# Kernel optimization log

Measured on AMD Instinct MI355X. Metric: run time of the kernel, lower is better.

Reference implementation:

```python
import jax, jax.numpy as jnp
import numpy as np

B, N, D = 8, 1024, 1024
H = 16
HD = D // H  # 64
SCALE = float(HD) ** -0.5


def setup_inputs() -> dict:
    key = jax.random.key(0)
    k1, k2, k3 = jax.random.split(key, 3)
    x = jax.random.normal(k1, (B, N, D), dtype=jnp.float32)
    W_qkv = jax.random.normal(k2, (D, 3 * D), dtype=jnp.float32) * (D ** -0.5)
    b_qkv = jnp.zeros((3 * D,), dtype=jnp.float32)
    W_o = jax.random.normal(k3, (D, D), dtype=jnp.float32) * (D ** -0.5)
    b_o = jnp.zeros((D,), dtype=jnp.float32)
    return {"x": x, "W_qkv": W_qkv, "b_qkv": b_qkv, "W_o": W_o, "b_o": b_o}


def reference(x, W_qkv, b_qkv, W_o, b_o):
    b, n, _ = x.shape
    qkv = x @ W_qkv + b_qkv                      # (B, N, 3D)
    qkv = qkv.reshape(b, n, H, 3 * HD).transpose(0, 2, 1, 3)  # (B, H, N, 3*HD)
    q, k, v = jnp.split(qkv, 3, axis=-1)          # each (B, H, N, HD)
    attn = jnp.einsum('bhnd,bhmd->bhnm', q, k) * SCALE
    attn = jax.nn.softmax(attn, axis=-1)          # (B, H, N, N); dropout p=0 -> identity
    heads = jnp.einsum('bhnm,bhmd->bhnd', attn, v)
    heads = heads.transpose(0, 2, 1, 3).reshape(b, n, H * HD)  # (B, N, D)
    return heads @ W_o + b_o
```

## Files before the change

### kernel.cpp

```cpp
#include <hip/hip_runtime.h>
#include <hip/hip_bf16.h>

typedef unsigned short ushort_t;
typedef __bf16 bf16x8 __attribute__((ext_vector_type(8)));
typedef float floatx4 __attribute__((ext_vector_type(4)));

#define MFMA(a, b, c) __builtin_amdgcn_mfma_f32_16x16x32_bf16(a, b, c, 0, 0, 0)

__device__ __forceinline__ float b2f(ushort_t u) {
    union { ushort_t u; __hip_bfloat16 h; } cvt; cvt.u = u; return __bfloat162float(cvt.h);
}
__device__ __forceinline__ ushort_t f2b(float f) {
    union { ushort_t u; __hip_bfloat16 h; } cvt; cvt.h = __float2bfloat16(f); return cvt.u;
}

__device__ __forceinline__ void async_copy16(const ushort_t* g, ushort_t* l) {
    __builtin_amdgcn_global_load_lds(
        (const __attribute__((address_space(1))) void*)g,
        (__attribute__((address_space(3))) void*)l, 16, 0, 0);
}

__global__ void convert_x(const float* __restrict__ xin, ushort_t* __restrict__ xb) {
    int i = blockIdx.x * 256 + threadIdx.x;
    const float4* xf = (const float4*)xin;
    float4 a = xf[i * 2], b = xf[i * 2 + 1];
    union { ushort_t s[8]; uint4 v; } p;
    p.s[0] = f2b(a.x); p.s[1] = f2b(a.y); p.s[2] = f2b(a.z); p.s[3] = f2b(a.w);
    p.s[4] = f2b(b.x); p.s[5] = f2b(b.y); p.s[6] = f2b(b.z); p.s[7] = f2b(b.w);
    ((uint4*)xb)[i] = p.v;
}

__global__ void transpose_cvt_qkv(const float* __restrict__ W, ushort_t* __restrict__ Wt) {
    __shared__ float tile[32][33];
    int p0 = blockIdx.x * 32, k0 = blockIdx.y * 32;
    int which = p0 >> 10, rem = p0 & 1023;
    int n0 = (rem >> 6) * 192 + which * 64 + (rem & 63);
    int tx = threadIdx.x, ty = threadIdx.y;
#pragma unroll
    for (int i = 0; i < 4; ++i)
        tile[ty + i * 8][tx] = W[(size_t)(k0 + ty + i * 8) * 3072 + n0 + tx];
    __syncthreads();
#pragma unroll
    for (int i = 0; i < 4; ++i)
        Wt[(size_t)(p0 + ty + i * 8) * 1024 + k0 + tx] = f2b(tile[tx][ty + i * 8]);
}

__global__ void transpose_cvt(const float* __restrict__ W, ushort_t* __restrict__ Wt,
                              int K, int N) {
    __shared__ float tile[32][33];
    int n0 = blockIdx.x * 32, k0 = blockIdx.y * 32;
    int tx = threadIdx.x, ty = threadIdx.y;
#pragma unroll
    for (int i = 0; i < 4; ++i)
        tile[ty + i * 8][tx] = W[(size_t)(k0 + ty + i * 8) * N + n0 + tx];
    __syncthreads();
#pragma unroll
    for (int i = 0; i < 4; ++i)
        Wt[(size_t)(n0 + ty + i * 8) * K + k0 + tx] = f2b(tile[tx][ty + i * 8]);
}

__device__ __forceinline__ int tswz(int n, int m) {
    return n * 128 + (((m >> 3) ^ (n & 15)) << 3) + (m & 7);
}

__global__ __launch_bounds__(256, 3) void gemm_qkv(
    const ushort_t* __restrict__ A,
    const ushort_t* __restrict__ Bt,
    const float* __restrict__ bias,
    ushort_t* __restrict__ Qb, ushort_t* __restrict__ Kb, ushort_t* __restrict__ Vtb) {
    const int K = 1024;
    __shared__ __align__(16) ushort_t SH[16384];
    ushort_t* Alds = SH;
    ushort_t* Blds = SH + 8192;
    int tid = threadIdx.x;
    int wave = tid >> 6, lane = tid & 63;
    int quad = lane >> 4, l16 = lane & 15;
    int wm = (wave >> 1) * 64, wn = (wave & 1) * 64;
    int m0 = blockIdx.x * 128, n0 = blockIdx.y * 128;

    floatx4 acc[4][4] = {};

    int srow[4], scol[4];
#pragma unroll
    for (int p = 0; p < 4; ++p) {
        int slot = (wave * 4 + p) * 64 + lane;
        int row = slot >> 3;
        srow[p] = row;
        scol[p] = ((slot & 7) ^ (row & 7)) * 8;
    }

    for (int kt = 0; kt < 16; ++kt) {
        int k0 = kt * 64;
        __syncthreads();
#pragma unroll
        for (int p = 0; p < 4; ++p) {
            int t = wave * 4 + p;
            async_copy16(&A[(m0 + srow[p]) * K + k0 + scol[p]], &Alds[t * 512]);
            async_copy16(&Bt[(n0 + srow[p]) * K + k0 + scol[p]], &Blds[t * 512]);
        }
        __syncthreads();
#pragma unroll
        for (int ki = 0; ki < 2; ++ki) {
            bf16x8 af[4], bfv[4];
            int sc = ((ki * 4 + quad) ^ (l16 & 7)) * 8;
#pragma unroll
            for (int i = 0; i < 4; ++i) {
                __builtin_memcpy(&af[i],  &Alds[(wm + i * 16 + l16) * 64 + sc], 16);
                __builtin_memcpy(&bfv[i], &Blds[(wn + i * 16 + l16) * 64 + sc], 16);
            }
#pragma unroll
            for (int i = 0; i < 4; ++i)
#pragma unroll
                for (int j = 0; j < 4; ++j)
                    acc[i][j] = MFMA(af[i], bfv[j], acc[i][j]);
        }
    }

    int which = n0 >> 10;
    int b = m0 >> 10;

    if (which < 2) {
        ushort_t* dst = which ? Kb : Qb;
        float sc = which ? 1.0f : 0.18033688f;
#pragma unroll
        for (int j = 0; j < 4; ++j) {
            int C = n0 + wn + j * 16 + l16;
            int c = C & 1023;
            int h = c >> 6, d = c & 63;
            float bv = bias[((C >> 6) & 15) * 192 + which * 64 + (C & 63)];
            size_t hb = (size_t)(b * 16 + h) * 65536 + d;
#pragma unroll
            for (int i = 0; i < 4; ++i)
#pragma unroll
                for (int g = 0; g < 4; ++g) {
                    int n_tok = (m0 & 1023) + wm + i * 16 + quad * 4 + g;
                    dst[hb + (size_t)n_tok * 64] = f2b((acc[i][j][g] + bv) * sc);
                }
        }
    } else {
        __syncthreads();
#pragma unroll
        for (int j = 0; j < 4; ++j) {
            int C = n0 + wn + j * 16 + l16;
            int nl = wn + j * 16 + l16;
            float bv = bias[((C >> 6) & 15) * 192 + 128 + (C & 63)];
#pragma unroll
            for (int i = 0; i < 4; ++i)
#pragma unroll
                for (int g = 0; g < 4; ++g) {
                    int ml = wm + i * 16 + quad * 4 + g;
                    SH[tswz(nl, ml)] = f2b(acc[i][j][g] + bv);
                }
        }
        __syncthreads();
        int r = tid >> 1, half = tid & 1;
        int vcol = (n0 - 2048) + r;
        int h = vcol >> 6, d = vcol & 63;
        size_t base = ((size_t)(b * 16 + h) * 64 + d) * 1024 + (m0 & 1023) + half * 64;
#pragma unroll
        for (int i8 = 0; i8 < 8; ++i8) {
            int chunk = half * 8 + i8;
            uint4 v;
            __builtin_memcpy(&v, &SH[r * 128 + ((chunk ^ (r & 15)) << 3)], 16);
            __builtin_memcpy(&Vtb[base + i8 * 8], &v, 16);
        }
    }
}

__global__ __launch_bounds__(256, 3) void attn(
    const ushort_t* __restrict__ Qb, const ushort_t* __restrict__ Kb,
    const ushort_t* __restrict__ Vtb, ushort_t* __restrict__ heads) {
    __shared__ __align__(16) ushort_t Klds[2][4096];
    __shared__ __align__(16) ushort_t Vlds[2][4096];
    __shared__ __align__(16) ushort_t Plds[128 * 76];
    int tid = threadIdx.x;
    int wave = tid >> 6, lane = tid & 63;
    int quad = lane >> 4, l16 = lane & 15;

    int slot = blockIdx.y + 16 * blockIdx.z;
    int bh = blockIdx.x + 8 * (slot >> 3);
    int qx = slot & 7;
    int b = bh >> 4, h = bh & 15;
    const ushort_t* Qh = Qb + (size_t)bh * 65536;
    const ushort_t* Kh = Kb + (size_t)bh * 65536;
    const ushort_t* Vh = Vtb + (size_t)bh * 65536;

    bf16x8 qa[2][2];
#pragma unroll
    for (int mi = 0; mi < 2; ++mi) {
        int qrow = qx * 128 + wave * 32 + mi * 16 + l16;
        __builtin_memcpy(&qa[mi][0], &Qh[qrow * 64 + quad * 8], 16);
        __builtin_memcpy(&qa[mi][1], &Qh[qrow * 64 + 32 + quad * 8], 16);
    }

    floatx4 oacc[2][4] = {};
    floatx4 oext[2] = {};

    bf16x8 onesfrag;
    {
        ushort_t v = (l16 == 0) ? (ushort_t)0x3F80 : (ushort_t)0;
        ushort_t tmp[8] = {v, v, v, v, v, v, v, v};
        __builtin_memcpy(&onesfrag, tmp, 16);
    }

    int srow[2], scol[2];
#pragma unroll
    for (int p = 0; p < 2; ++p) {
        int slot2 = (wave * 2 + p) * 64 + lane;
        int row = slot2 >> 3;
        srow[p] = row;
        scol[p] = ((slot2 & 7) ^ (row & 7)) * 8;
    }

#pragma unroll
    for (int p = 0; p < 2; ++p) {
        int t = wave * 2 + p;
        async_copy16(&Kh[srow[p] * 64 + scol[p]], &Klds[0][t * 512]);
        async_copy16(&Vh[srow[p] * 1024 + scol[p]], &Vlds[0][t * 512]);
    }

    for (int kt = 0; kt < 16; ++kt) {
        int cur = kt & 1;
        __syncthreads();
        if (kt < 15) {
            int nk0 = (kt + 1) * 64, nb = cur ^ 1;
#pragma unroll
            for (int p = 0; p < 2; ++p) {
                int t = wave * 2 + p;
                async_copy16(&Kh[(nk0 + srow[p]) * 64 + scol[p]], &Klds[nb][t * 512]);
                async_copy16(&Vh[srow[p] * 1024 + nk0 + scol[p]], &Vlds[nb][t * 512]);
            }
        }

        bf16x8 kf[4][2];
#pragma unroll
        for (int n = 0; n < 4; ++n)
#pragma unroll
            for (int ki = 0; ki < 2; ++ki) {
                int sc = ((ki * 4 + quad) ^ (l16 & 7)) * 8;
                __builtin_memcpy(&kf[n][ki], &Klds[cur][(n * 16 + l16) * 64 + sc], 16);
            }
#pragma unroll
        for (int mi = 0; mi < 2; ++mi)
#pragma unroll
            for (int n = 0; n < 4; ++n) {
                floatx4 z = {0.f, 0.f, 0.f, 0.f};
#pragma unroll
                for (int ki = 0; ki < 2; ++ki)
                    z = MFMA(kf[n][ki], qa[mi][ki], z);
                union { ushort_t s[4]; double d8; } pk;
#pragma unroll
                for (int g = 0; g < 4; ++g)
                    pk.s[g] = f2b(__builtin_exp2f(z[g]));
                __builtin_memcpy(
                    &Plds[(wave * 32 + mi * 16 + l16) * 76 + n * 16 + quad * 4],
                    &pk, 8);
            }

        bf16x8 vf[4][2];
#pragma unroll
        for (int n = 0; n < 4; ++n)
#pragma unroll
            for (int ki = 0; ki < 2; ++ki) {
                int sc = ((ki * 4 + quad) ^ (l16 & 7)) * 8;
                __builtin_memcpy(&vf[n][ki], &Vlds[cur][(n * 16 + l16) * 64 + sc], 16);
            }
#pragma unroll
        for (int mi = 0; mi < 2; ++mi) {
            bf16x8 pa[2];
            int prow = wave * 32 + mi * 16 + l16;
#pragma unroll
            for (int ki = 0; ki < 2; ++ki)
                __builtin_memcpy(&pa[ki], &Plds[prow * 76 + ki * 32 + quad * 8], 16);
            __builtin_amdgcn_s_setprio(1);
#pragma unroll
            for (int n = 0; n < 4; ++n)
#pragma unroll
                for (int ki = 0; ki < 2; ++ki)
                    oacc[mi][n] = MFMA(pa[ki], vf[n][ki], oacc[mi][n]);
#pragma unroll
            for (int ki = 0; ki < 2; ++ki)
                oext[mi] = MFMA(pa[ki], onesfrag, oext[mi]);
            __builtin_amdgcn_s_setprio(0);
        }
    }

#pragma unroll
    for (int mi = 0; mi < 2; ++mi)
#pragma unroll
        for (int g = 0; g < 4; ++g) {
            float l = __shfl(oext[mi][g], (lane & 48));
            float inv = 1.f / l;
            int n_tok = qx * 128 + wave * 32 + mi * 16 + quad * 4 + g;
#pragma unroll
            for (int n = 0; n < 4; ++n)
                heads[(size_t)(b * 1024 + n_tok) * 1024 + h * 64 + n * 16 + l16] =
                    f2b(oacc[mi][n][g] * inv);
        }
}

__global__ __launch_bounds__(256, 3) void gemm_out(
    const ushort_t* __restrict__ A,
    const ushort_t* __restrict__ Bt,
    const float* __restrict__ bias,
    float* __restrict__ out) {
    const int K = 1024;
    __shared__ __align__(16) ushort_t Alds[128 * 64];
    __shared__ __align__(16) ushort_t Blds[128 * 64];
    int tid = threadIdx.x;
    int wave = tid >> 6, lane = tid & 63;
    int quad = lane >> 4, l16 = lane & 15;
    int wm = (wave >> 1) * 64, wn = (wave & 1) * 64;
    int m0 = blockIdx.x * 128, n0 = blockIdx.y * 128;

    floatx4 acc[4][4] = {};

    int srow[4], scol[4];
#pragma unroll
    for (int p = 0; p < 4; ++p) {
        int slot = (wave * 4 + p) * 64 + lane;
        int row = slot >> 3;
        srow[p] = row;
        scol[p] = ((slot & 7) ^ (row & 7)) * 8;
    }

    for (int kt = 0; kt < 16; ++kt) {
        int k0 = kt * 64;
        __syncthreads();
#pragma unroll
        for (int p = 0; p < 4; ++p) {
            int t = wave * 4 + p;
            async_copy16(&A[(m0 + srow[p]) * K + k0 + scol[p]], &Alds[t * 512]);
            async_copy16(&Bt[(n0 + srow[p]) * K + k0 + scol[p]], &Blds[t * 512]);
        }
        __syncthreads();
#pragma unroll
        for (int ki = 0; ki < 2; ++ki) {
            bf16x8 af[4], bfv[4];
            int sc = ((ki * 4 + quad) ^ (l16 & 7)) * 8;
#pragma unroll
            for (int i = 0; i < 4; ++i) {
                __builtin_memcpy(&af[i],  &Alds[(wm + i * 16 + l16) * 64 + sc], 16);
                __builtin_memcpy(&bfv[i], &Blds[(wn + i * 16 + l16) * 64 + sc], 16);
            }
#pragma unroll
            for (int i = 0; i < 4; ++i)
#pragma unroll
                for (int j = 0; j < 4; ++j)
                    acc[i][j] = MFMA(af[i], bfv[j], acc[i][j]);
        }
    }

#pragma unroll
    for (int j = 0; j < 4; ++j) {
        int C = n0 + wn + j * 16 + l16;
        float bv = bias[C];
#pragma unroll
        for (int i = 0; i < 4; ++i)
#pragma unroll
            for (int g = 0; g < 4; ++g) {
                int R = m0 + wm + i * 16 + quad * 4 + g;
                out[(size_t)R * 1024 + C] = acc[i][j][g] + bv;
            }
    }
}

extern "C" void kernel_launch(void* const* d_in, const int* in_sizes, int n_in,
                              void* d_out, int out_size, void* d_ws, size_t ws_size,
                              hipStream_t stream) {
    const float* x    = (const float*)d_in[0];
    const float* Wqkv = (const float*)d_in[1];
    const float* bqkv = (const float*)d_in[2];
    const float* Wo   = (const float*)d_in[3];
    const float* bo   = (const float*)d_in[4];

    char* ws = (char*)d_ws;
    const size_t MB = 1u << 20;
    ushort_t* xb    = (ushort_t*)(ws);
    ushort_t* Qb    = (ushort_t*)(ws + 16 * MB);
    ushort_t* Kb    = (ushort_t*)(ws + 32 * MB);
    ushort_t* Vtb   = (ushort_t*)(ws + 48 * MB);
    ushort_t* heads = (ushort_t*)(ws + 64 * MB);
    ushort_t* WqkvT = (ushort_t*)(ws + 64 * MB);
    ushort_t* WoT   = (ushort_t*)(ws);

    convert_x<<<4096, 256, 0, stream>>>(x, xb);
    transpose_cvt_qkv<<<dim3(96, 32), dim3(32, 8), 0, stream>>>(Wqkv, WqkvT);
    gemm_qkv<<<dim3(64, 24), 256, 0, stream>>>(xb, WqkvT, bqkv, Qb, Kb, Vtb);
    attn<<<dim3(8, 16, 8), 256, 0, stream>>>(Qb, Kb, Vtb, heads);
    transpose_cvt<<<dim3(32, 32), dim3(32, 8), 0, stream>>>(Wo, WoT, 1024, 1024);
    gemm_out<<<dim3(64, 8), 256, 0, stream>>>(heads, WoT, bo, (float*)d_out);
}
```

Measured before the change: 242.9 us.

## Merge prep kernels, remap GEMM block order, single-buffer attention, raise occupancy

Folds the x conversion and both weight transpose/convert kernels into one prep launch, which removes two kernel launches and allows the Wo transpose to run before the GEMMs. It also remaps the GEMM block indices so that neighbouring blocks share tiles for L2 reuse. The attention kernel drops K/V double buffering and adds a second barrier per tile, halving its LDS use so that launch bounds can target 4 blocks per CU. The risk is that the async K/V loads are no longer overlapped with compute inside each block, which shifts latency hiding onto higher occupancy.

```diff
diff --git a/kernel.cpp b/kernel.cpp
--- a/kernel.cpp
+++ b/kernel.cpp
@@ -20,50 +20,51 @@
         (__attribute__((address_space(3))) void*)l, 16, 0, 0);
 }
 
-__global__ void convert_x(const float* __restrict__ xin, ushort_t* __restrict__ xb) {
-    int i = blockIdx.x * 256 + threadIdx.x;
-    const float4* xf = (const float4*)xin;
-    float4 a = xf[i * 2], b = xf[i * 2 + 1];
-    union { ushort_t s[8]; uint4 v; } p;
-    p.s[0] = f2b(a.x); p.s[1] = f2b(a.y); p.s[2] = f2b(a.z); p.s[3] = f2b(a.w);
-    p.s[4] = f2b(b.x); p.s[5] = f2b(b.y); p.s[6] = f2b(b.z); p.s[7] = f2b(b.w);
-    ((uint4*)xb)[i] = p.v;
-}
-
-__global__ void transpose_cvt_qkv(const float* __restrict__ W, ushort_t* __restrict__ Wt) {
+__global__ void prep(const float* __restrict__ xin, ushort_t* __restrict__ xb,
+                     const float* __restrict__ Wqkv, ushort_t* __restrict__ WqkvT,
+                     const float* __restrict__ Wo, ushort_t* __restrict__ WoT) {
     __shared__ float tile[32][33];
-    int p0 = blockIdx.x * 32, k0 = blockIdx.y * 32;
-    int which = p0 >> 10, rem = p0 & 1023;
-    int n0 = (rem >> 6) * 192 + which * 64 + (rem & 63);
-    int tx = threadIdx.x, ty = threadIdx.y;
-#pragma unroll
-    for (int i = 0; i < 4; ++i)
-        tile[ty + i * 8][tx] = W[(size_t)(k0 + ty + i * 8) * 3072 + n0 + tx];
-    __syncthreads();
-#pragma unroll
-    for (int i = 0; i < 4; ++i)
-        Wt[(size_t)(p0 + ty + i * 8) * 1024 + k0 + tx] = f2b(tile[tx][ty + i * 8]);
-}
-
-__global__ void transpose_cvt(const float* __restrict__ W, ushort_t* __restrict__ Wt,
-                              int K, int N) {
-    __shared__ float tile[32][33];
-    int n0 = blockIdx.x * 32, k0 = blockIdx.y * 32;
-    int tx = threadIdx.x, ty = threadIdx.y;
-#pragma unroll
-    for (int i = 0; i < 4; ++i)
-        tile[ty + i * 8][tx] = W[(size_t)(k0 + ty + i * 8) * N + n0 + tx];
-    __syncthreads();
-#pragma unroll
-    for (int i = 0; i < 4; ++i)
-        Wt[(size_t)(n0 + ty + i * 8) * K + k0 + tx] = f2b(tile[tx][ty + i * 8]);
+    int bb = blockIdx.x;
+    if (bb < 4096) {
+        int i = bb * 256 + threadIdx.x;
+        const float4* xf = (const float4*)xin;
+        float4 a = xf[i * 2], b = xf[i * 2 + 1];
+        union { ushort_t s[8]; uint4 v; } p;
+        p.s[0] = f2b(a.x); p.s[1] = f2b(a.y); p.s[2] = f2b(a.z); p.s[3] = f2b(a.w);
+        p.s[4] = f2b(b.x); p.s[5] = f2b(b.y); p.s[6] = f2b(b.z); p.s[7] = f2b(b.w);
+        ((uint4*)xb)[i] = p.v;
+    } else if (bb < 7168) {
+        int b2 = bb - 4096;
+        int p0 = (b2 % 96) * 32, k0 = (b2 / 96) * 32;
+        int which = p0 >> 10, rem = p0 & 1023;
+        int n0 = (rem >> 6) * 192 + which * 64 + (rem & 63);
+        int tx = threadIdx.x & 31, ty = threadIdx.x >> 5;
+#pragma unroll
+        for (int i = 0; i < 4; ++i)
+            tile[ty + i * 8][tx] = Wqkv[(size_t)(k0 + ty + i * 8) * 3072 + n0 + tx];
+        __syncthreads();
+#pragma unroll
+        for (int i = 0; i < 4; ++i)
+            WqkvT[(size_t)(p0 + ty + i * 8) * 1024 + k0 + tx] = f2b(tile[tx][ty + i * 8]);
+    } else {
+        int b3 = bb - 7168;
+        int n0 = (b3 & 31) * 32, k0 = (b3 >> 5) * 32;
+        int tx = threadIdx.x & 31, ty = threadIdx.x >> 5;
+#pragma unroll
+        for (int i = 0; i < 4; ++i)
+            tile[ty + i * 8][tx] = Wo[(size_t)(k0 + ty + i * 8) * 1024 + n0 + tx];
+        __syncthreads();
+#pragma unroll
+        for (int i = 0; i < 4; ++i)
+            WoT[(size_t)(n0 + ty + i * 8) * 1024 + k0 + tx] = f2b(tile[tx][ty + i * 8]);
+    }
 }
 
 __device__ __forceinline__ int tswz(int n, int m) {
     return n * 128 + (((m >> 3) ^ (n & 15)) << 3) + (m & 7);
 }
 
-__global__ __launch_bounds__(256, 3) void gemm_qkv(
+__global__ __launch_bounds__(256, 4) void gemm_qkv(
     const ushort_t* __restrict__ A,
     const ushort_t* __restrict__ Bt,
     const float* __restrict__ bias,
@@ -76,7 +77,10 @@
     int wave = tid >> 6, lane = tid & 63;
     int quad = lane >> 4, l16 = lane & 15;
     int wm = (wave >> 1) * 64, wn = (wave & 1) * 64;
-    int m0 = blockIdx.x * 128, n0 = blockIdx.y * 128;
+
+    int lin = blockIdx.x + 64 * blockIdx.y;
+    int nl = (lin & 7) * 192 + (lin >> 3);
+    int m0 = (nl & 63) * 128, n0 = (nl >> 6) * 128;
 
     floatx4 acc[4][4] = {};
 
@@ -142,14 +146,14 @@
 #pragma unroll
         for (int j = 0; j < 4; ++j) {
             int C = n0 + wn + j * 16 + l16;
-            int nl = wn + j * 16 + l16;
+            int nl2 = wn + j * 16 + l16;
             float bv = bias[((C >> 6) & 15) * 192 + 128 + (C & 63)];
 #pragma unroll
             for (int i = 0; i < 4; ++i)
 #pragma unroll
                 for (int g = 0; g < 4; ++g) {
                     int ml = wm + i * 16 + quad * 4 + g;
-                    SH[tswz(nl, ml)] = f2b(acc[i][j][g] + bv);
+                    SH[tswz(nl2, ml)] = f2b(acc[i][j][g] + bv);
                 }
         }
         __syncthreads();
@@ -167,11 +171,11 @@
     }
 }
 
-__global__ __launch_bounds__(256, 3) void attn(
+__global__ __launch_bounds__(256, 4) void attn(
     const ushort_t* __restrict__ Qb, const ushort_t* __restrict__ Kb,
     const ushort_t* __restrict__ Vtb, ushort_t* __restrict__ heads) {
-    __shared__ __align__(16) ushort_t Klds[2][4096];
-    __shared__ __align__(16) ushort_t Vlds[2][4096];
+    __shared__ __align__(16) ushort_t Klds[4096];
+    __shared__ __align__(16) ushort_t Vlds[4096];
     __shared__ __align__(16) ushort_t Plds[128 * 76];
     int tid = threadIdx.x;
     int wave = tid >> 6, lane = tid & 63;
@@ -212,25 +216,16 @@
         scol[p] = ((slot2 & 7) ^ (row & 7)) * 8;
     }
 
-#pragma unroll
-    for (int p = 0; p < 2; ++p) {
-        int t = wave * 2 + p;
-        async_copy16(&Kh[srow[p] * 64 + scol[p]], &Klds[0][t * 512]);
-        async_copy16(&Vh[srow[p] * 1024 + scol[p]], &Vlds[0][t * 512]);
-    }
-
     for (int kt = 0; kt < 16; ++kt) {
-        int cur = kt & 1;
-        __syncthreads();
-        if (kt < 15) {
-            int nk0 = (kt + 1) * 64, nb = cur ^ 1;
-#pragma unroll
-            for (int p = 0; p < 2; ++p) {
-                int t = wave * 2 + p;
-                async_copy16(&Kh[(nk0 + srow[p]) * 64 + scol[p]], &Klds[nb][t * 512]);
-                async_copy16(&Vh[srow[p] * 1024 + nk0 + scol[p]], &Vlds[nb][t * 512]);
-            }
-        }
+        int k0 = kt * 64;
+        __syncthreads();
+#pragma unroll
+        for (int p = 0; p < 2; ++p) {
+            int t = wave * 2 + p;
+            async_copy16(&Kh[(k0 + srow[p]) * 64 + scol[p]], &Klds[t * 512]);
+            async_copy16(&Vh[srow[p] * 1024 + k0 + scol[p]], &Vlds[t * 512]);
+        }
+        __syncthreads();
 
         bf16x8 kf[4][2];
 #pragma unroll
@@ -238,7 +233,7 @@
 #pragma unroll
             for (int ki = 0; ki < 2; ++ki) {
                 int sc = ((ki * 4 + quad) ^ (l16 & 7)) * 8;
-                __builtin_memcpy(&kf[n][ki], &Klds[cur][(n * 16 + l16) * 64 + sc], 16);
+                __builtin_memcpy(&kf[n][ki], &Klds[(n * 16 + l16) * 64 + sc], 16);
             }
 #pragma unroll
         for (int mi = 0; mi < 2; ++mi)
@@ -263,7 +258,7 @@
 #pragma unroll
             for (int ki = 0; ki < 2; ++ki) {
                 int sc = ((ki * 4 + quad) ^ (l16 & 7)) * 8;
-                __builtin_memcpy(&vf[n][ki], &Vlds[cur][(n * 16 + l16) * 64 + sc], 16);
+                __builtin_memcpy(&vf[n][ki], &Vlds[(n * 16 + l16) * 64 + sc], 16);
             }
 #pragma unroll
         for (int mi = 0; mi < 2; ++mi) {
@@ -299,7 +294,7 @@
         }
 }
 
-__global__ __launch_bounds__(256, 3) void gemm_out(
+__global__ __launch_bounds__(256, 4) void gemm_out(
     const ushort_t* __restrict__ A,
     const ushort_t* __restrict__ Bt,
     const float* __restrict__ bias,
@@ -311,7 +306,10 @@
     int wave = tid >> 6, lane = tid & 63;
     int quad = lane >> 4, l16 = lane & 15;
     int wm = (wave >> 1) * 64, wn = (wave & 1) * 64;
-    int m0 = blockIdx.x * 128, n0 = blockIdx.y * 128;
+
+    int lin = blockIdx.x + 64 * blockIdx.y;
+    int nl = (lin & 7) * 64 + (lin >> 3);
+    int m0 = (nl & 63) * 128, n0 = (nl >> 6) * 128;
 
     floatx4 acc[4][4] = {};
 
@@ -380,14 +378,12 @@
     ushort_t* Qb    = (ushort_t*)(ws + 16 * MB);
     ushort_t* Kb    = (ushort_t*)(ws + 32 * MB);
     ushort_t* Vtb   = (ushort_t*)(ws + 48 * MB);
-    ushort_t* heads = (ushort_t*)(ws + 64 * MB);
     ushort_t* WqkvT = (ushort_t*)(ws + 64 * MB);
-    ushort_t* WoT   = (ushort_t*)(ws);
-
-    convert_x<<<4096, 256, 0, stream>>>(x, xb);
-    transpose_cvt_qkv<<<dim3(96, 32), dim3(32, 8), 0, stream>>>(Wqkv, WqkvT);
+    ushort_t* WoT   = (ushort_t*)(ws + 70 * MB);
+    ushort_t* heads = (ushort_t*)(ws);
+
+    prep<<<8192, 256, 0, stream>>>(x, xb, Wqkv, WqkvT, Wo, WoT);
     gemm_qkv<<<dim3(64, 24), 256, 0, stream>>>(xb, WqkvT, bqkv, Qb, Kb, Vtb);
     attn<<<dim3(8, 16, 8), 256, 0, stream>>>(Qb, Kb, Vtb, heads);
-    transpose_cvt<<<dim3(32, 32), dim3(32, 8), 0, stream>>>(Wo, WoT, 1024, 1024);
     gemm_out<<<dim3(64, 8), 256, 0, stream>>>(heads, WoT, bo, (float*)d_out);
 }
```

Result: slower. 256.7 us (+5.7%).
